# Performance work log

Measured on AMD Instinct MI355X. Metric: run time of the kernel, lower is better.

The kernel has to match this reference:

```python
import jax, jax.numpy as jnp
import numpy as np

B = 128   # batch (== seq_len, required by the original indexing)
S = 128   # seq_len
H = 512   # hidden_size == embed_dim == LSTM input size
HH = 256  # hidden_size // 2 (per-direction hidden)
L = 2     # n_layers
V = 30000 # vocab for each record embedding table


def setup_inputs() -> dict:
    key = jax.random.key(0)
    ks = jax.random.split(key, 12)
    rt = jax.random.randint(ks[0], (B, S), 0, V)
    re = jax.random.randint(ks[1], (B, S), 0, V)
    rm = jax.random.randint(ks[2], (B, S), 0, V)
    h0 = jnp.zeros((2 * L, HH), jnp.float32)  # pytorch layout: index = layer*2 + direction
    c0 = jnp.zeros((2 * L, HH), jnp.float32)
    E_rt = jax.random.normal(ks[3], (V, H), jnp.float32) * 0.02
    E_re = jax.random.normal(ks[4], (V, H), jnp.float32) * 0.02
    E_rm = jax.random.normal(ks[5], (V, H), jnp.float32) * 0.02
    k = 1.0 / np.sqrt(HH)
    Wih = jax.random.uniform(ks[6], (L, 2, 4 * HH, H), jnp.float32, -k, k)
    Whh = jax.random.uniform(ks[7], (L, 2, 4 * HH, HH), jnp.float32, -k, k)
    bih = jax.random.uniform(ks[8], (L, 2, 4 * HH), jnp.float32, -k, k)
    bhh = jax.random.uniform(ks[9], (L, 2, 4 * HH), jnp.float32, -k, k)
    return {"rt": rt, "re": re, "rm": rm, "h0": h0, "c0": c0,
            "E_rt": E_rt, "E_re": E_re, "E_rm": E_rm,
            "Wih": Wih, "Whh": Whh, "bih": bih, "bhh": bhh}


def _lstm_dir(x, h0, c0, wih, whh, b, reverse):
    # x: (S, in_dim); pytorch gate order i, f, g, o
    def step(carry, xt):
        h, c = carry
        g = xt @ wih.T + h @ whh.T + b  # (4*HH,)
        i, f, gg, o = jnp.split(g, 4, axis=-1)
        c = jax.nn.sigmoid(f) * c + jax.nn.sigmoid(i) * jnp.tanh(gg)
        h = jax.nn.sigmoid(o) * jnp.tanh(c)
        return (h, c), h
    (hN, cN), ys = jax.lax.scan(step, (h0, c0), x, reverse=reverse)
    return ys, hN, cN


def reference(rt, re, rm, h0, c0, E_rt, E_re, E_rm, Wih, Whh, bih, bhh):
    emb = E_rt[rt] + E_re[re] + E_rm[rm]  # (B, S, H)
    b = bih + bhh

    def per_sample(xseq, h, c):
        # full 2-layer bidirectional LSTM over one sample's sequence (batch=1 in original)
        inp = xseq
        hs, cs = [], []
        for l in range(L):
            yf, hf, cf = _lstm_dir(inp, h[2 * l],     c[2 * l],     Wih[l, 0], Whh[l, 0], b[l, 0], False)
            yb, hb, cb = _lstm_dir(inp, h[2 * l + 1], c[2 * l + 1], Wih[l, 1], Whh[l, 1], b[l, 1], True)
            inp = jnp.concatenate([yf, yb], axis=-1)  # (S, H)
            hs += [hf, hb]; cs += [cf, cb]
        return inp, jnp.stack(hs), jnp.stack(cs)

    def sample_step(carry, xs):
        h, c = carry
        ei, xseq = xs
        reset = (ei > 0) & (ei % 32 == 0)  # periodic hidden reset across samples
        h = jnp.where(reset, jnp.zeros_like(h), h)
        c = jnp.where(reset, jnp.zeros_like(c), c)
        out, hN, cN = per_sample(xseq, h, c)
        return (hN, cN), out

    (_, _), bilstm_outs = jax.lax.scan(sample_step, (h0, c0), (jnp.arange(emb.shape[0]), emb))
    # original: permute(1,2,0) then max_pool1d over last dim == max over the loop (sample) axis
    output = bilstm_outs.max(axis=0)  # (S, H)
    return bilstm_outs, output
```

## Files before the change

kernel.cpp:

```cpp
#include <hip/hip_runtime.h>
#include <hip/hip_bf16.h>


typedef _Float16 f16;
typedef _Float16 h2_t  __attribute__((ext_vector_type(2)));
typedef _Float16 f16x8 __attribute__((ext_vector_type(8)));
typedef float    f32x4 __attribute__((ext_vector_type(4)));

#define B_  128
#define S_  128
#define H_  512
#define HH_ 256
#define M_  (B_ * S_)
#define NG  1024
#define K0  512

#define WS_BASE 106971200u
#define WS_PIPE 106972224u

__device__ __forceinline__ float sigmoidf_(float x) { return 1.0f / (1.0f + __expf(-x)); }
__device__ __forceinline__ float tanhf_(float x)    { return 1.0f - 2.0f / (__expf(2.0f * x) + 1.0f); }

__device__ __forceinline__ float ldf(const void* p, long i, int isbf) {
    return isbf ? __bfloat162float(((const __hip_bfloat16*)p)[i]) : ((const float*)p)[i];
}

__device__ __forceinline__ float dot2f(int w, int h, float acc) {
#if __has_builtin(__builtin_amdgcn_fdot2)
    return __builtin_amdgcn_fdot2(__builtin_bit_cast(h2_t, w), __builtin_bit_cast(h2_t, h), acc, false);
#else
    h2_t a = __builtin_bit_cast(h2_t, w), b = __builtin_bit_cast(h2_t, h);
    return acc + (float)a[0] * (float)b[0] + (float)a[1] * (float)b[1];
#endif
}

template <int SLP>
__device__ __forceinline__ void block_wait_ge(int* p, int v) {
    if (threadIdx.x == 0) {
        while (__hip_atomic_load(p, __ATOMIC_RELAXED, __HIP_MEMORY_SCOPE_AGENT) < v)
            __builtin_amdgcn_s_sleep(SLP);
        (void)__hip_atomic_load(p, __ATOMIC_ACQUIRE, __HIP_MEMORY_SCOPE_AGENT);
    }
    __syncthreads();
}
__device__ __forceinline__ void block_release(int* p) {
    if (threadIdx.x == 0) {
        __threadfence();
        __hip_atomic_fetch_add(p, 1, __ATOMIC_RELEASE, __HIP_MEMORY_SCOPE_AGENT);
    }
}

struct SmemRecur {
    f16    hbuf[2][256];
    int4   wlds4[2][2][8][256];
    float2 plds[256];
};
struct SmemWorker {
    f16 As[128][72];
    f16 Bs[256][72];
};
union PipeSmem { SmemRecur r; SmemWorker w; };

__global__ void k_detect(const unsigned short* __restrict__ e, int* __restrict__ flag) {
    __shared__ int cnt;
    if (threadIdx.x == 0) cnt = 0;
    __syncthreads();
    unsigned short v = e[threadIdx.x];
    int ex = (v >> 7) & 0xFF;
    if (ex >= 100 && ex < 127) atomicAdd(&cnt, 1);
    __syncthreads();
    if (threadIdx.x == 0) *flag = (cnt >= 200) ? 1 : 0;
}

__global__ void k_zero(int* __restrict__ flags) { flags[threadIdx.x] = 0; }

__global__ void k_embed(const int* __restrict__ rt, const int* __restrict__ re, const int* __restrict__ rm,
                        const void* __restrict__ Ert, const void* __restrict__ Ere,
                        const void* __restrict__ Erm, f16* __restrict__ emb,
                        const int* __restrict__ flag) {
    const int isbf = *flag;
    int gid = blockIdx.x * 256 + threadIdx.x;
    int bs = gid >> 9, h = gid & 511;
    float v = ldf(Ert, (long)rt[bs] * H_ + h, isbf)
            + ldf(Ere, (long)re[bs] * H_ + h, isbf)
            + ldf(Erm, (long)rm[bs] * H_ + h, isbf);
    emb[gid] = (f16)v;
}

__global__ void k_wconv(const void* __restrict__ Wih, const void* __restrict__ Whh,
                        const void* __restrict__ bih, const void* __restrict__ bhh,
                        f16* __restrict__ wih, f16* __restrict__ whh, float* __restrict__ bias,
                        const int* __restrict__ flag) {
    const int isbf = *flag;
    int gid = blockIdx.x * 256 + threadIdx.x;
    wih[gid] = (f16)ldf(Wih, gid, isbf);
    if (gid < 1048576) whh[gid] = (f16)ldf(Whh, gid, isbf);
    if (gid < 4096)    bias[gid] = ldf(bih, gid, isbf) + ldf(bhh, gid, isbf);
}

__global__ __launch_bounds__(256) void k_gemm(const f16* __restrict__ A, const f16* __restrict__ Bm,
                                              f16* __restrict__ C) {
    const int bm = blockIdx.x & 127;
    const int bn = blockIdx.x >> 7;
    const int tid = threadIdx.x;
    const int lane = tid & 63, wave = tid >> 6;
    const int wm = wave & 1, wn = wave >> 1;
    __shared__ __align__(16) f16 As[128][72];
    __shared__ __align__(16) f16 Bs[128][72];
    f32x4 acc[4][4];
#pragma unroll
    for (int i = 0; i < 4; ++i)
#pragma unroll
        for (int jj = 0; jj < 4; ++jj) acc[i][jj] = (f32x4){0.f, 0.f, 0.f, 0.f};
    const long abase = (long)bm * 128 * K0;
    const long bbase = (long)bn * 128 * K0;
    for (int kt = 0; kt < K0; kt += 64) {
#pragma unroll
        for (int p = 0; p < 4; ++p) {
            int r = p * 32 + (tid >> 3), s = tid & 7;
            *(int4*)&As[r][s * 8] = *(const int4*)(A  + abase + (long)r * K0 + kt + s * 8);
            *(int4*)&Bs[r][s * 8] = *(const int4*)(Bm + bbase + (long)r * K0 + kt + s * 8);
        }
        __syncthreads();
        const int quad = lane >> 4, l15 = lane & 15;
#pragma unroll
        for (int kc = 0; kc < 64; kc += 32) {
            f16x8 af[4], bf[4];
#pragma unroll
            for (int mt = 0; mt < 4; ++mt) af[mt] = *(const f16x8*)&As[wm * 64 + mt * 16 + l15][kc + quad * 8];
#pragma unroll
            for (int nt = 0; nt < 4; ++nt) bf[nt] = *(const f16x8*)&Bs[wn * 64 + nt * 16 + l15][kc + quad * 8];
#pragma unroll
            for (int mt = 0; mt < 4; ++mt)
#pragma unroll
                for (int nt = 0; nt < 4; ++nt)
                    acc[mt][nt] = __builtin_amdgcn_mfma_f32_16x16x32_f16(af[mt], bf[nt], acc[mt][nt], 0, 0, 0);
        }
        __syncthreads();
    }
    const int quad = lane >> 4, l15 = lane & 15;
#pragma unroll
    for (int mt = 0; mt < 4; ++mt)
#pragma unroll
        for (int nt = 0; nt < 4; ++nt)
#pragma unroll
            for (int r = 0; r < 4; ++r) {
                int row = bm * 128 + wm * 64 + mt * 16 + quad * 4 + r;
                int col = bn * 128 + wn * 64 + nt * 16 + l15;
                C[(long)row * 2048 + col] = (f16)acc[mt][nt][r];
            }
}

__device__ void recur_body(PipeSmem* SM,
    const f16* __restrict__ xp, const f16* __restrict__ whh, const float* __restrict__ bias,
    const void* __restrict__ h0, const void* __restrict__ c0,
    f16* __restrict__ yf16, void* __restrict__ yout,
    int layer, int isbf, int q, int d, int* rel, int* acq) {

    const int tid = threadIdx.x;
    const int j = tid & 255, half = tid >> 8;
    const int G0 = half * 2, G1 = G0 + 1;
    const int ld = layer * 2 + d;
    const f16* wrow0 = whh + (long)ld * NG * 256;

    SmemRecur& S = SM->r;

    int4 w4[2][24];
    {
        const int4* r0 = (const int4*)(wrow0 + (long)(G0 * 256 + j) * 256);
        const int4* r1 = (const int4*)(wrow0 + (long)(G1 * 256 + j) * 256);
#pragma unroll
        for (int c = 0; c < 24; ++c) { w4[0][c] = r0[c]; w4[1][c] = r1[c]; }
#pragma unroll
        for (int c = 0; c < 8; ++c) {
            S.wlds4[half][0][c][j] = r0[24 + c];
            S.wlds4[half][1][c][j] = r1[24 + c];
        }
    }
    const float b0 = bias[ld * NG + G0 * 256 + j];
    const float b1 = bias[ld * NG + G1 * 256 + j];

    float cst = 0.f;
    if (half == 0) {
        float hv = 0.f;
        if (q == 0) {
            cst = ldf(c0, ld * 256 + j, isbf);
            hv  = ldf(h0, ld * 256 + j, isbf);
        }
        S.hbuf[0][j] = (f16)hv;
    }
    __syncthreads();

    int cur = 0;
    for (int i = 0; i < 32; ++i) {
        const int b = q * 32 + i;
        if (acq) block_wait_ge<2>(&acq[b], 2);
        for (int ti = 0; ti < 128; ++ti) {
            const int t = d ? (127 - ti) : ti;
            const f16* xr = xp + ((long)b * 128 + t) * 2048 + d * NG + j;
            f16 px0h = xr[G0 * 256];
            f16 px1h = xr[G1 * 256];

            float a0 = b0, a1 = b1;
            const int4* hp = (const int4*)S.hbuf[cur];
#pragma unroll
            for (int blk = 0; blk < 6; ++blk) {
                int4 hh[4];
#pragma unroll
                for (int u = 0; u < 4; ++u) hh[u] = hp[blk * 4 + u];
#pragma unroll
                for (int u = 0; u < 4; ++u) {
                    int4 wa = w4[0][blk * 4 + u], wb = w4[1][blk * 4 + u];
                    a0 = dot2f(wa.x, hh[u].x, a0); a0 = dot2f(wa.y, hh[u].y, a0);
                    a0 = dot2f(wa.z, hh[u].z, a0); a0 = dot2f(wa.w, hh[u].w, a0);
                    a1 = dot2f(wb.x, hh[u].x, a1); a1 = dot2f(wb.y, hh[u].y, a1);
                    a1 = dot2f(wb.z, hh[u].z, a1); a1 = dot2f(wb.w, hh[u].w, a1);
                }
            }
#pragma unroll
            for (int c = 0; c < 8; ++c) {
                int4 hh = hp[24 + c];
                int4 wa = S.wlds4[half][0][c][j];
                int4 wb = S.wlds4[half][1][c][j];
                a0 = dot2f(wa.x, hh.x, a0); a0 = dot2f(wa.y, hh.y, a0);
                a0 = dot2f(wa.z, hh.z, a0); a0 = dot2f(wa.w, hh.w, a0);
                a1 = dot2f(wb.x, hh.x, a1); a1 = dot2f(wb.y, hh.y, a1);
                a1 = dot2f(wb.z, hh.z, a1); a1 = dot2f(wb.w, hh.w, a1);
            }
            a0 += (float)px0h;
            a1 += (float)px1h;

            if (half) S.plds[j] = make_float2(a0, a1);
            __syncthreads();
            if (!half) {
                float2 go = S.plds[j];
                float ig = sigmoidf_(a0);
                float fg = sigmoidf_(a1);
                float gg = tanhf_(go.x);
                float og = sigmoidf_(go.y);
                cst = fg * cst + ig * gg;
                float hn = og * tanhf_(cst);
                S.hbuf[cur ^ 1][j] = (f16)hn;
                long oidx = ((long)b * 128 + t) * 512 + d * 256 + j;
                if (layer == 0) {
                    yf16[oidx] = (f16)hn;
                } else {
                    if (isbf) ((__hip_bfloat16*)yout)[oidx] = __float2bfloat16(hn);
                    else      ((float*)yout)[oidx] = hn;
                }
            }
            cur ^= 1;
            __syncthreads();
        }
        if (rel) block_release(&rel[b]);
    }
}

__device__ void worker_body(PipeSmem* SM, const f16* __restrict__ y0, const f16* __restrict__ wih1,
                            f16* __restrict__ xpb, int* flags, int wid) {
    SmemWorker& S = SM->w;
    const int tid = threadIdx.x;
    const int lane = tid & 63, wave = tid >> 6;
    const int wm = wave & 1, wn = wave >> 1;
    const int quad = lane >> 4, l15 = lane & 15;

    for (int m = wid; m < 256; m += 32) {
        const int i = m >> 3, q = (m >> 1) & 3, h2 = m & 1;
        const int b = q * 32 + i;
        block_wait_ge<32>(&flags[b], 2);
        for (int slab = 0; slab < 4; ++slab) {
            const int n0 = h2 * 1024 + slab * 256;
            f32x4 acc[4][4];
#pragma unroll
            for (int a = 0; a < 4; ++a)
#pragma unroll
                for (int c = 0; c < 4; ++c) acc[a][c] = (f32x4){0.f, 0.f, 0.f, 0.f};
            for (int kt = 0; kt < 512; kt += 64) {
#pragma unroll
                for (int p = 0; p < 2; ++p) {
                    int r = p * 64 + (tid >> 3), s = tid & 7;
                    *(int4*)&S.As[r][s * 8] = *(const int4*)(y0 + ((long)(b * 128 + r)) * 512 + kt + s * 8);
                }
#pragma unroll
                for (int p = 0; p < 4; ++p) {
                    int r = p * 64 + (tid >> 3), s = tid & 7;
                    *(int4*)&S.Bs[r][s * 8] = *(const int4*)(wih1 + ((long)(n0 + r)) * 512 + kt + s * 8);
                }
                __syncthreads();
#pragma unroll
                for (int kc = 0; kc < 64; kc += 32) {
                    f16x8 af[4], bf[4];
#pragma unroll
                    for (int mt = 0; mt < 4; ++mt) af[mt] = *(const f16x8*)&S.As[wm * 64 + mt * 16 + l15][kc + quad * 8];
#pragma unroll
                    for (int nt = 0; nt < 4; ++nt) bf[nt] = *(const f16x8*)&S.Bs[wn * 64 + nt * 16 + l15][kc + quad * 8];
#pragma unroll
                    for (int mt = 0; mt < 4; ++mt)
#pragma unroll
                        for (int nt = 0; nt < 4; ++nt)
                            acc[mt][nt] = __builtin_amdgcn_mfma_f32_16x16x32_f16(af[mt], bf[nt], acc[mt][nt], 0, 0, 0);
                }
                __syncthreads();
            }
#pragma unroll
            for (int mt = 0; mt < 4; ++mt)
#pragma unroll
                for (int nt = 0; nt < 4; ++nt)
#pragma unroll
                    for (int r = 0; r < 4; ++r) {
                        int row = b * 128 + wm * 64 + mt * 16 + quad * 4 + r;
                        int col = n0 + wn * 64 + nt * 16 + l15;
                        xpb[(long)row * 2048 + col] = (f16)acc[mt][nt][r];
                    }
        }
        __syncthreads();
        block_release(&flags[128 + b]);
    }
}

__global__ __launch_bounds__(512, 1) void k_pipe(
    f16* __restrict__ xpb, const f16* __restrict__ whh, const float* __restrict__ bias,
    const void* __restrict__ h0, const void* __restrict__ c0,
    f16* __restrict__ y0, void* __restrict__ yout, const f16* __restrict__ wih1,
    int* __restrict__ flags, const int* __restrict__ flag) {
    __shared__ __align__(16) PipeSmem SM;
    const int blk = blockIdx.x;
    if (blk < 8) {
        recur_body(&SM, xpb, whh, bias, h0, c0, y0, yout, 0, *flag, blk >> 1, blk & 1, flags, nullptr);
    } else if (blk < 40) {
        worker_body(&SM, y0, wih1, xpb, flags, blk - 8);
    } else {
        const int r = blk - 40;
        recur_body(&SM, xpb, whh, bias, h0, c0, y0, yout, 1, *flag, r >> 1, r & 1, nullptr, flags + 128);
    }
}

__global__ __launch_bounds__(512, 1) void k_recur_solo(
    const f16* __restrict__ xp, const f16* __restrict__ whh, const float* __restrict__ bias,
    const void* __restrict__ h0, const void* __restrict__ c0,
    f16* __restrict__ yf16, void* __restrict__ yout, int layer, const int* __restrict__ flag) {
    __shared__ __align__(16) PipeSmem SM;
    recur_body(&SM, xp, whh, bias, h0, c0, yf16, yout, layer, *flag,
               blockIdx.x >> 1, blockIdx.x & 1, nullptr, nullptr);
}

__global__ void k_maxpool(const void* __restrict__ bil, void* __restrict__ outbase,
                          const int* __restrict__ flag) {
    const int isbf = *flag;
    int gid = blockIdx.x * 256 + threadIdx.x;
    float m = -1e30f;
    for (int b = 0; b < 128; ++b)
        m = fmaxf(m, ldf(bil, (long)b * 65536 + gid, isbf));
    long o = (long)M_ * H_ + gid;
    if (isbf) ((__hip_bfloat16*)outbase)[o] = __float2bfloat16(m);
    else      ((float*)outbase)[o] = m;
}

extern "C" void kernel_launch(void* const* d_in, const int* in_sizes, int n_in,
                              void* d_out, int out_size, void* d_ws, size_t ws_size,
                              hipStream_t stream) {
    const int* rt = (const int*)d_in[0];
    const int* re = (const int*)d_in[1];
    const int* rm = (const int*)d_in[2];
    const void* h0  = d_in[3];
    const void* c0  = d_in[4];
    const void* Ert = d_in[5];
    const void* Ere = d_in[6];
    const void* Erm = d_in[7];
    const void* Wih = d_in[8];
    const void* Whh = d_in[9];
    const void* bih = d_in[10];
    const void* bhh = d_in[11];

    if (ws_size < WS_BASE) return;
    const bool pipe = (ws_size >= WS_PIPE);

    char* ws = (char*)d_ws;
    f16*   emb  = (f16*)(ws);
    f16*   wih  = (f16*)(ws + 16777216);
    f16*   whh  = (f16*)(ws + 20971520);
    float* bias = (float*)(ws + 23068672);
    f16*   xpb  = (f16*)(ws + 23085056);
    f16*   y0   = (f16*)(ws + 90193920);
    int*   flag = (int*)(ws + 106971136);
    int*   flags= (int*)(ws + 106971200);

    hipLaunchKernelGGL(k_detect, dim3(1),     dim3(256), 0, stream, (const unsigned short*)Ert, flag);
    hipLaunchKernelGGL(k_embed,  dim3(32768), dim3(256), 0, stream, rt, re, rm, Ert, Ere, Erm, emb, flag);
    hipLaunchKernelGGL(k_wconv,  dim3(8192),  dim3(256), 0, stream, Wih, Whh, bih, bhh, wih, whh, bias, flag);
    hipLaunchKernelGGL(k_gemm,   dim3(2048),  dim3(256), 0, stream, emb, wih, xpb);
    if (pipe) {
        hipLaunchKernelGGL(k_zero, dim3(1),   dim3(256), 0, stream, flags);
        hipLaunchKernelGGL(k_pipe, dim3(48),  dim3(512), 0, stream,
                           xpb, whh, bias, h0, c0, y0, d_out, wih + (long)2 * NG * K0, flags, flag);
    } else {
        hipLaunchKernelGGL(k_recur_solo, dim3(8), dim3(512), 0, stream, xpb, whh, bias, h0, c0, y0, d_out, 0, flag);
        hipLaunchKernelGGL(k_gemm,  dim3(2048), dim3(256), 0, stream, y0, wih + (long)2 * NG * K0, xpb);
        hipLaunchKernelGGL(k_recur_solo, dim3(8), dim3(512), 0, stream, xpb, whh, bias, h0, c0, y0, d_out, 1, flag);
    }
    hipLaunchKernelGGL(k_maxpool, dim3(256),  dim3(256), 0, stream, d_out, d_out, flag);
}
```

Before: 8.794 ms.

## Compute all four LSTM gates per thread with 256-thread recurrence blocks

The recurrent step now uses 256 threads per block, and each thread computes all four gate dot products for one hidden unit. This removes the cross-half exchange through shared memory and one __syncthreads per timestep. Most of Whh is held in registers (26 of 32 int4 chunks per gate row) and the rest in LDS. The layer-1 input GEMM in the workers is split into 128x128 tiles with a finer work granularity, and the consumer wait count is raised to 16 to match. The trade-off is much higher register pressure (104 int4 of weights per thread) and fewer threads available to hide latency.

```diff
diff --git a/kernel.cpp b/kernel.cpp
--- a/kernel.cpp
+++ b/kernel.cpp
@@ -51,13 +51,12 @@
 }
 
 struct SmemRecur {
-    f16    hbuf[2][256];
-    int4   wlds4[2][2][8][256];
-    float2 plds[256];
+    int4 wlds[4][6][256];
+    f16  hbuf[2][256];
 };
 struct SmemWorker {
     f16 As[128][72];
-    f16 Bs[256][72];
+    f16 Bs[128][72];
 };
 union PipeSmem { SmemRecur r; SmemWorker w; };
 
@@ -157,97 +156,88 @@
     f16* __restrict__ yf16, void* __restrict__ yout,
     int layer, int isbf, int q, int d, int* rel, int* acq) {
 
-    const int tid = threadIdx.x;
-    const int j = tid & 255, half = tid >> 8;
-    const int G0 = half * 2, G1 = G0 + 1;
+    const int j = threadIdx.x;
     const int ld = layer * 2 + d;
-    const f16* wrow0 = whh + (long)ld * NG * 256;
-
     SmemRecur& S = SM->r;
 
-    int4 w4[2][24];
-    {
-        const int4* r0 = (const int4*)(wrow0 + (long)(G0 * 256 + j) * 256);
-        const int4* r1 = (const int4*)(wrow0 + (long)(G1 * 256 + j) * 256);
-#pragma unroll
-        for (int c = 0; c < 24; ++c) { w4[0][c] = r0[c]; w4[1][c] = r1[c]; }
-#pragma unroll
-        for (int c = 0; c < 8; ++c) {
-            S.wlds4[half][0][c][j] = r0[24 + c];
-            S.wlds4[half][1][c][j] = r1[24 + c];
-        }
-    }
-    const float b0 = bias[ld * NG + G0 * 256 + j];
-    const float b1 = bias[ld * NG + G1 * 256 + j];
-
-    float cst = 0.f;
-    if (half == 0) {
-        float hv = 0.f;
-        if (q == 0) {
-            cst = ldf(c0, ld * 256 + j, isbf);
-            hv  = ldf(h0, ld * 256 + j, isbf);
-        }
-        S.hbuf[0][j] = (f16)hv;
-    }
+    int4 wreg[4][26];
+#pragma unroll
+    for (int tt = 0; tt < 4; ++tt) {
+        const int4* r = (const int4*)(whh + ((long)ld * NG + tt * 256 + j) * 256);
+#pragma unroll
+        for (int c = 0; c < 26; ++c) wreg[tt][c] = r[c];
+#pragma unroll
+        for (int c = 0; c < 6; ++c)  S.wlds[tt][c][j] = r[26 + c];
+    }
+    float bs0 = bias[ld * NG +   0 + j];
+    float bs1 = bias[ld * NG + 256 + j];
+    float bs2 = bias[ld * NG + 512 + j];
+    float bs3 = bias[ld * NG + 768 + j];
+
+    float cst = 0.f, hv = 0.f;
+    if (q == 0) {
+        cst = ldf(c0, ld * 256 + j, isbf);
+        hv  = ldf(h0, ld * 256 + j, isbf);
+    }
+    S.hbuf[0][j] = (f16)hv;
     __syncthreads();
 
     int cur = 0;
     for (int i = 0; i < 32; ++i) {
         const int b = q * 32 + i;
-        if (acq) block_wait_ge<2>(&acq[b], 2);
+        if (acq) block_wait_ge<2>(&acq[b], 16);
         for (int ti = 0; ti < 128; ++ti) {
             const int t = d ? (127 - ti) : ti;
             const f16* xr = xp + ((long)b * 128 + t) * 2048 + d * NG + j;
-            f16 px0h = xr[G0 * 256];
-            f16 px1h = xr[G1 * 256];
-
-            float a0 = b0, a1 = b1;
+            f16 p0 = xr[0];
+            f16 p1 = xr[256];
+            f16 p2 = xr[512];
+            f16 p3 = xr[768];
+
+            float a0 = bs0, a1 = bs1, a2 = bs2, a3 = bs3;
             const int4* hp = (const int4*)S.hbuf[cur];
 #pragma unroll
-            for (int blk = 0; blk < 6; ++blk) {
-                int4 hh[4];
-#pragma unroll
-                for (int u = 0; u < 4; ++u) hh[u] = hp[blk * 4 + u];
-#pragma unroll
-                for (int u = 0; u < 4; ++u) {
-                    int4 wa = w4[0][blk * 4 + u], wb = w4[1][blk * 4 + u];
-                    a0 = dot2f(wa.x, hh[u].x, a0); a0 = dot2f(wa.y, hh[u].y, a0);
-                    a0 = dot2f(wa.z, hh[u].z, a0); a0 = dot2f(wa.w, hh[u].w, a0);
-                    a1 = dot2f(wb.x, hh[u].x, a1); a1 = dot2f(wb.y, hh[u].y, a1);
-                    a1 = dot2f(wb.z, hh[u].z, a1); a1 = dot2f(wb.w, hh[u].w, a1);
-                }
-            }
-#pragma unroll
-            for (int c = 0; c < 8; ++c) {
-                int4 hh = hp[24 + c];
-                int4 wa = S.wlds4[half][0][c][j];
-                int4 wb = S.wlds4[half][1][c][j];
-                a0 = dot2f(wa.x, hh.x, a0); a0 = dot2f(wa.y, hh.y, a0);
-                a0 = dot2f(wa.z, hh.z, a0); a0 = dot2f(wa.w, hh.w, a0);
-                a1 = dot2f(wb.x, hh.x, a1); a1 = dot2f(wb.y, hh.y, a1);
-                a1 = dot2f(wb.z, hh.z, a1); a1 = dot2f(wb.w, hh.w, a1);
-            }
-            a0 += (float)px0h;
-            a1 += (float)px1h;
-
-            if (half) S.plds[j] = make_float2(a0, a1);
-            __syncthreads();
-            if (!half) {
-                float2 go = S.plds[j];
-                float ig = sigmoidf_(a0);
-                float fg = sigmoidf_(a1);
-                float gg = tanhf_(go.x);
-                float og = sigmoidf_(go.y);
-                cst = fg * cst + ig * gg;
-                float hn = og * tanhf_(cst);
-                S.hbuf[cur ^ 1][j] = (f16)hn;
-                long oidx = ((long)b * 128 + t) * 512 + d * 256 + j;
-                if (layer == 0) {
-                    yf16[oidx] = (f16)hn;
-                } else {
-                    if (isbf) ((__hip_bfloat16*)yout)[oidx] = __float2bfloat16(hn);
-                    else      ((float*)yout)[oidx] = hn;
-                }
+            for (int c = 0; c < 26; ++c) {
+                int4 hh = hp[c];
+                int4 w0 = wreg[0][c], w1 = wreg[1][c], w2 = wreg[2][c], w3 = wreg[3][c];
+                a0 = dot2f(w0.x, hh.x, a0); a0 = dot2f(w0.y, hh.y, a0);
+                a0 = dot2f(w0.z, hh.z, a0); a0 = dot2f(w0.w, hh.w, a0);
+                a1 = dot2f(w1.x, hh.x, a1); a1 = dot2f(w1.y, hh.y, a1);
+                a1 = dot2f(w1.z, hh.z, a1); a1 = dot2f(w1.w, hh.w, a1);
+                a2 = dot2f(w2.x, hh.x, a2); a2 = dot2f(w2.y, hh.y, a2);
+                a2 = dot2f(w2.z, hh.z, a2); a2 = dot2f(w2.w, hh.w, a2);
+                a3 = dot2f(w3.x, hh.x, a3); a3 = dot2f(w3.y, hh.y, a3);
+                a3 = dot2f(w3.z, hh.z, a3); a3 = dot2f(w3.w, hh.w, a3);
+            }
+#pragma unroll
+            for (int c = 0; c < 6; ++c) {
+                int4 hh = hp[26 + c];
+                int4 w0 = S.wlds[0][c][j], w1 = S.wlds[1][c][j];
+                int4 w2 = S.wlds[2][c][j], w3 = S.wlds[3][c][j];
+                a0 = dot2f(w0.x, hh.x, a0); a0 = dot2f(w0.y, hh.y, a0);
+                a0 = dot2f(w0.z, hh.z, a0); a0 = dot2f(w0.w, hh.w, a0);
+                a1 = dot2f(w1.x, hh.x, a1); a1 = dot2f(w1.y, hh.y, a1);
+                a1 = dot2f(w1.z, hh.z, a1); a1 = dot2f(w1.w, hh.w, a1);
+                a2 = dot2f(w2.x, hh.x, a2); a2 = dot2f(w2.y, hh.y, a2);
+                a2 = dot2f(w2.z, hh.z, a2); a2 = dot2f(w2.w, hh.w, a2);
+                a3 = dot2f(w3.x, hh.x, a3); a3 = dot2f(w3.y, hh.y, a3);
+                a3 = dot2f(w3.z, hh.z, a3); a3 = dot2f(w3.w, hh.w, a3);
+            }
+            a0 += (float)p0; a1 += (float)p1; a2 += (float)p2; a3 += (float)p3;
+
+            float ig = sigmoidf_(a0);
+            float fg = sigmoidf_(a1);
+            float gg = tanhf_(a2);
+            float og = sigmoidf_(a3);
+            cst = fg * cst + ig * gg;
+            float hn = og * tanhf_(cst);
+            S.hbuf[cur ^ 1][j] = (f16)hn;
+            long oidx = ((long)b * 128 + t) * 512 + d * 256 + j;
+            if (layer == 0) {
+                yf16[oidx] = (f16)hn;
+            } else {
+                if (isbf) ((__hip_bfloat16*)yout)[oidx] = __float2bfloat16(hn);
+                else      ((float*)yout)[oidx] = hn;
             }
             cur ^= 1;
             __syncthreads();
@@ -264,61 +254,56 @@
     const int wm = wave & 1, wn = wave >> 1;
     const int quad = lane >> 4, l15 = lane & 15;
 
-    for (int m = wid; m < 256; m += 32) {
-        const int i = m >> 3, q = (m >> 1) & 3, h2 = m & 1;
-        const int b = q * 32 + i;
+    for (int e = wid; e < 2048; e += 32) {
+        const int ii = e >> 6, rem = e & 63, q = rem >> 4, n = rem & 15;
+        const int b = q * 32 + ii;
         block_wait_ge<32>(&flags[b], 2);
-        for (int slab = 0; slab < 4; ++slab) {
-            const int n0 = h2 * 1024 + slab * 256;
-            f32x4 acc[4][4];
-#pragma unroll
-            for (int a = 0; a < 4; ++a)
-#pragma unroll
-                for (int c = 0; c < 4; ++c) acc[a][c] = (f32x4){0.f, 0.f, 0.f, 0.f};
-            for (int kt = 0; kt < 512; kt += 64) {
-#pragma unroll
-                for (int p = 0; p < 2; ++p) {
-                    int r = p * 64 + (tid >> 3), s = tid & 7;
-                    *(int4*)&S.As[r][s * 8] = *(const int4*)(y0 + ((long)(b * 128 + r)) * 512 + kt + s * 8);
+        const long abase = (long)b * 128 * K0;
+        const long bbase = (long)n * 128 * K0;
+        f32x4 acc[4][4];
+#pragma unroll
+        for (int a = 0; a < 4; ++a)
+#pragma unroll
+            for (int c = 0; c < 4; ++c) acc[a][c] = (f32x4){0.f, 0.f, 0.f, 0.f};
+        for (int kt = 0; kt < K0; kt += 64) {
+#pragma unroll
+            for (int p = 0; p < 4; ++p) {
+                int r = p * 32 + (tid >> 3), s = tid & 7;
+                *(int4*)&S.As[r][s * 8] = *(const int4*)(y0   + abase + (long)r * K0 + kt + s * 8);
+                *(int4*)&S.Bs[r][s * 8] = *(const int4*)(wih1 + bbase + (long)r * K0 + kt + s * 8);
+            }
+            __syncthreads();
+#pragma unroll
+            for (int kc = 0; kc < 64; kc += 32) {
+                f16x8 af[4], bf[4];
+#pragma unroll
+                for (int mt = 0; mt < 4; ++mt) af[mt] = *(const f16x8*)&S.As[wm * 64 + mt * 16 + l15][kc + quad * 8];
+#pragma unroll
+                for (int nt = 0; nt < 4; ++nt) bf[nt] = *(const f16x8*)&S.Bs[wn * 64 + nt * 16 + l15][kc + quad * 8];
+#pragma unroll
+                for (int mt = 0; mt < 4; ++mt)
+#pragma unroll
+                    for (int nt = 0; nt < 4; ++nt)
+                        acc[mt][nt] = __builtin_amdgcn_mfma_f32_16x16x32_f16(af[mt], bf[nt], acc[mt][nt], 0, 0, 0);
+            }
+            __syncthreads();
+        }
+#pragma unroll
+        for (int mt = 0; mt < 4; ++mt)
+#pragma unroll
+            for (int nt = 0; nt < 4; ++nt)
+#pragma unroll
+                for (int r = 0; r < 4; ++r) {
+                    int row = b * 128 + wm * 64 + mt * 16 + quad * 4 + r;
+                    int col = n * 128 + wn * 64 + nt * 16 + l15;
+                    xpb[(long)row * 2048 + col] = (f16)acc[mt][nt][r];
                 }
-#pragma unroll
-                for (int p = 0; p < 4; ++p) {
-                    int r = p * 64 + (tid >> 3), s = tid & 7;
-                    *(int4*)&S.Bs[r][s * 8] = *(const int4*)(wih1 + ((long)(n0 + r)) * 512 + kt + s * 8);
-                }
-                __syncthreads();
-#pragma unroll
-                for (int kc = 0; kc < 64; kc += 32) {
-                    f16x8 af[4], bf[4];
-#pragma unroll
-                    for (int mt = 0; mt < 4; ++mt) af[mt] = *(const f16x8*)&S.As[wm * 64 + mt * 16 + l15][kc + quad * 8];
-#pragma unroll
-                    for (int nt = 0; nt < 4; ++nt) bf[nt] = *(const f16x8*)&S.Bs[wn * 64 + nt * 16 + l15][kc + quad * 8];
-#pragma unroll
-                    for (int mt = 0; mt < 4; ++mt)
-#pragma unroll
-                        for (int nt = 0; nt < 4; ++nt)
-                            acc[mt][nt] = __builtin_amdgcn_mfma_f32_16x16x32_f16(af[mt], bf[nt], acc[mt][nt], 0, 0, 0);
-                }
-                __syncthreads();
-            }
-#pragma unroll
-            for (int mt = 0; mt < 4; ++mt)
-#pragma unroll
-                for (int nt = 0; nt < 4; ++nt)
-#pragma unroll
-                    for (int r = 0; r < 4; ++r) {
-                        int row = b * 128 + wm * 64 + mt * 16 + quad * 4 + r;
-                        int col = n0 + wn * 64 + nt * 16 + l15;
-                        xpb[(long)row * 2048 + col] = (f16)acc[mt][nt][r];
-                    }
-        }
         __syncthreads();
         block_release(&flags[128 + b]);
     }
 }
 
-__global__ __launch_bounds__(512, 1) void k_pipe(
+__global__ __launch_bounds__(256, 1) void k_pipe(
     f16* __restrict__ xpb, const f16* __restrict__ whh, const float* __restrict__ bias,
     const void* __restrict__ h0, const void* __restrict__ c0,
     f16* __restrict__ y0, void* __restrict__ yout, const f16* __restrict__ wih1,
@@ -335,7 +320,7 @@
     }
 }
 
-__global__ __launch_bounds__(512, 1) void k_recur_solo(
+__global__ __launch_bounds__(256, 1) void k_recur_solo(
     const f16* __restrict__ xp, const f16* __restrict__ whh, const float* __restrict__ bias,
     const void* __restrict__ h0, const void* __restrict__ c0,
     f16* __restrict__ yf16, void* __restrict__ yout, int layer, const int* __restrict__ flag) {
@@ -391,12 +376,12 @@
     hipLaunchKernelGGL(k_gemm,   dim3(2048),  dim3(256), 0, stream, emb, wih, xpb);
     if (pipe) {
         hipLaunchKernelGGL(k_zero, dim3(1),   dim3(256), 0, stream, flags);
-        hipLaunchKernelGGL(k_pipe, dim3(48),  dim3(512), 0, stream,
+        hipLaunchKernelGGL(k_pipe, dim3(48),  dim3(256), 0, stream,
                            xpb, whh, bias, h0, c0, y0, d_out, wih + (long)2 * NG * K0, flags, flag);
     } else {
-        hipLaunchKernelGGL(k_recur_solo, dim3(8), dim3(512), 0, stream, xpb, whh, bias, h0, c0, y0, d_out, 0, flag);
+        hipLaunchKernelGGL(k_recur_solo, dim3(8), dim3(256), 0, stream, xpb, whh, bias, h0, c0, y0, d_out, 0, flag);
         hipLaunchKernelGGL(k_gemm,  dim3(2048), dim3(256), 0, stream, y0, wih + (long)2 * NG * K0, xpb);
-        hipLaunchKernelGGL(k_recur_solo, dim3(8), dim3(512), 0, stream, xpb, whh, bias, h0, c0, y0, d_out, 1, flag);
+        hipLaunchKernelGGL(k_recur_solo, dim3(8), dim3(256), 0, stream, xpb, whh, bias, h0, c0, y0, d_out, 1, flag);
     }
     hipLaunchKernelGGL(k_maxpool, dim3(256),  dim3(256), 0, stream, d_out, d_out, flag);
 }
```

Result: slower. 15.71 ms (+78.7%).
